# Optimization experiments

Measured on AMD Instinct MI355X. Metric: run time of the kernel, lower is better.

The kernel has to match this reference:

```python
import jax, jax.numpy as jnp
import numpy as np

N_POL = 100000
N_TICK = 20000
N = N_POL + N_TICK
E = 1000000
POL_FEAT = 7
EMB = 128
HID = 256
OUT = 128
N_STATES = 60


def setup_inputs() -> dict:
    key = jax.random.key(0)
    ks = jax.random.split(key, 16)
    s = 0.05
    return {
        "pol_features": jax.random.normal(ks[0], (N_POL, POL_FEAT), dtype=jnp.float32),
        "state_ids": jax.random.randint(ks[1], (N_POL,), 0, N_STATES, dtype=jnp.int32),
        "edge_index": jax.random.randint(ks[2], (2, E), 0, N, dtype=jnp.int32),
        "edge_weight": jax.random.uniform(ks[3], (E,), dtype=jnp.float32),
        # parameters
        "W_proj": jax.random.normal(ks[4], (POL_FEAT, EMB), dtype=jnp.float32) * s,
        "b_proj": jnp.zeros((EMB,), dtype=jnp.float32),
        "state_emb": jax.random.normal(ks[5], (N_STATES, EMB), dtype=jnp.float32) * s,
        "emb_tick": jax.random.normal(ks[6], (N_TICK, EMB), dtype=jnp.float32) * s,
        "W1_rel": jax.random.normal(ks[7], (EMB, HID), dtype=jnp.float32) * s,
        "b1_rel": jnp.zeros((HID,), dtype=jnp.float32),
        "W1_root": jax.random.normal(ks[8], (EMB, HID), dtype=jnp.float32) * s,
        "W2_rel": jax.random.normal(ks[9], (HID, OUT), dtype=jnp.float32) * s,
        "b2_rel": jnp.zeros((OUT,), dtype=jnp.float32),
        "W2_root": jax.random.normal(ks[10], (HID, OUT), dtype=jnp.float32) * s,
    }


def _graph_conv(x, edge_index, edge_weight, W_rel, b_rel, W_root):
    # PyG GraphConv: out = lin_rel(sum_{j->i} w_ji * x_j) + lin_root(x_i)
    src, dst = edge_index[0], edge_index[1]
    msg = x[src] * edge_weight[:, None]            # [E, d]
    agg = jax.ops.segment_sum(msg, dst, num_segments=N)  # [N, d]
    return agg @ W_rel + b_rel + x @ W_root


def reference(pol_features, state_ids, edge_index, edge_weight,
              W_proj, b_proj, state_emb, emb_tick,
              W1_rel, b1_rel, W1_root, W2_rel, b2_rel, W2_root):
    # Node features: projected politician feats + state embedding, cat tick embeddings
    pol = jax.nn.relu(pol_features @ W_proj + b_proj) + state_emb[state_ids]  # [N_POL, EMB]
    x = jnp.concatenate([pol, emb_tick], axis=0)   # [N, EMB]
    h = jax.nn.relu(_graph_conv(x, edge_index, edge_weight, W1_rel, b1_rel, W1_root))
    # dropout is identity in eval mode
    out = _graph_conv(h, edge_index, edge_weight, W2_rel, b2_rel, W2_root)
    return out  # [N, OUT]
```

## Files before the change

### kernel.cpp

```cpp
#include <hip/hip_runtime.h>
#include <hip/hip_bf16.h>

typedef unsigned short u16;
using short8  = __attribute__((ext_vector_type(8))) short;
using ushort8 = __attribute__((ext_vector_type(8))) unsigned short;
using float4v = __attribute__((ext_vector_type(4))) float;

#define N_POL  100000
#define N_TICK 20000
#define NNODE  120000
#define NEDGE  1000000
#define NTILE  1875
#define GB2    512

static __device__ __forceinline__ float b2f(u16 u) {
    return __uint_as_float(((unsigned)u) << 16);
}
static __device__ __forceinline__ u16 f2b(float f) {
    unsigned u = __float_as_uint(f);
    unsigned r = (u + 0x7FFFu + ((u >> 16) & 1u)) >> 16;
    return (u16)r;
}
static __device__ __forceinline__ float lde(const void* p, size_t i, int f32) {
    return f32 ? ((const float*)p)[i] : b2f(((const u16*)p)[i]);
}

static __device__ __forceinline__ size_t frag_addr(int k, int n) {
    return ((size_t)((n >> 4) * 8 + (k >> 5)) * 64 + (((k >> 3) & 3) * 16 + (n & 15))) * 8
           + (k & 7);
}

static __device__ __forceinline__ void gload_lds16(const u16* g, u16* l) {
    __builtin_amdgcn_global_load_lds(
        (const __attribute__((address_space(1))) void*)g,
        (__attribute__((address_space(3))) void*)l, 16, 0, 0);
}

static __device__ __forceinline__ void stage_tile(const u16* __restrict__ agg,
                                                  const u16* __restrict__ Xb,
                                                  int row0, u16* dst,
                                                  int wid, int lane) {
    int kqL = lane & 31;
#pragma unroll
    for (int i = 0; i < 8; i++) {
        int t = i * 4 + wid;
        int row = 2 * t + (lane >> 5);
        int kqG = kqL ^ (row & 7);
        const u16* src = (kqG < 16)
            ? agg + ((size_t)(row0 + row)) * 128 + kqG * 8
            : Xb + ((size_t)(row0 + row)) * 128 + (kqG - 16) * 8;
        gload_lds16(src, dst + (size_t)t * 512);
    }
}

__global__ void detect_k(const void* __restrict__ ew, int* __restrict__ flag) {
    if (threadIdx.x == 0) {
        const u16* p = (const u16*)ew;
        int huge = 0, allz = 1;
        for (int i = 0; i < 128; i += 2) {
            u16 b = p[i];
            if (b != 0) allz = 0;
            float v = b2f(b);
            if (!(fabsf(v) <= 4.0f)) huge = 1;
        }
        *flag = huge | allz;
    }
}

__global__ __launch_bounds__(256) void build_x(const void* __restrict__ pf,
                                               const int* __restrict__ sid,
                                               const void* __restrict__ Wp,
                                               const void* __restrict__ bp,
                                               const void* __restrict__ semb,
                                               const void* __restrict__ et,
                                               const int* __restrict__ flag,
                                               u16* __restrict__ Xb) {
    const int f32 = *flag;
    if (blockIdx.x < N_POL / 2) {
        int row = blockIdx.x * 2 + (threadIdx.x >> 7);
        int j = threadIdx.x & 127;
        float s = lde(bp, j, f32);
#pragma unroll
        for (int k = 0; k < 7; k++)
            s = fmaf(lde(pf, (size_t)row * 7 + k, f32), lde(Wp, k * 128 + j, f32), s);
        s = fmaxf(s, 0.f);
        s += lde(semb, (size_t)sid[row] * 128 + j, f32);
        Xb[(size_t)row * 128 + j] = f2b(s);
    } else {
        int idx = (blockIdx.x - N_POL / 2) * 256 + threadIdx.x;
        Xb[(size_t)N_POL * 128 + idx] = f2b(lde(et, idx, f32));
    }
}

__global__ __launch_bounds__(256) void prep_wf(const void* __restrict__ W1rel,
                                               const void* __restrict__ W1root,
                                               const void* __restrict__ W2rel,
                                               const void* __restrict__ W2root,
                                               const int* __restrict__ flag,
                                               u16* __restrict__ Wf1,
                                               u16* __restrict__ Wf2) {
    const int f32 = *flag;
    int idx = blockIdx.x * 256 + threadIdx.x;
    int id = idx & 65535;
    int k = id >> 8, n = id & 255;
    if (idx < 65536) {
        float v = (k < 128) ? lde(W1rel, (size_t)k * 256 + n, f32)
                            : lde(W1root, (size_t)(k - 128) * 256 + n, f32);
        Wf1[frag_addr(k, n)] = f2b(v);
    } else {
        float v = (n < 128) ? lde(W2rel, (size_t)k * 128 + n, f32)
                            : lde(W2root, (size_t)k * 128 + (n - 128), f32);
        Wf2[frag_addr(k, n)] = f2b(v);
    }
}

__global__ __launch_bounds__(256) void hist_dst(const int* __restrict__ ei,
                                                int* __restrict__ count,
                                                int* __restrict__ rank) {
    int e = blockIdx.x * 256 + threadIdx.x;
    if (e < NEDGE) rank[e] = atomicAdd(&count[ei[NEDGE + e]], 1);
}

__global__ __launch_bounds__(256) void scan1(const int* __restrict__ count,
                                             int* __restrict__ row_tmp,
                                             int* __restrict__ bsum) {
    __shared__ int sd[256];
    int t = threadIdx.x;
    int i = blockIdx.x * 256 + t;
    int c = (i < NNODE) ? count[i] : 0;
    sd[t] = c;
    __syncthreads();
#pragma unroll
    for (int off = 1; off < 256; off <<= 1) {
        int v = (t >= off) ? sd[t - off] : 0;
        __syncthreads();
        sd[t] += v;
        __syncthreads();
    }
    if (i < NNODE) row_tmp[i] = sd[t] - c;
    if (t == 255) bsum[blockIdx.x] = sd[t];
}

__global__ __launch_bounds__(512) void scan2(int* __restrict__ bsum, int nb) {
    __shared__ int sd[512];
    int t = threadIdx.x;
    int v = (t < nb) ? bsum[t] : 0;
    sd[t] = v;
    __syncthreads();
#pragma unroll
    for (int off = 1; off < 512; off <<= 1) {
        int u = (t >= off) ? sd[t - off] : 0;
        __syncthreads();
        sd[t] += u;
        __syncthreads();
    }
    if (t < nb) bsum[t] = sd[t] - v;
}

__global__ __launch_bounds__(256) void scan3(const int* __restrict__ row_tmp,
                                             const int* __restrict__ bsum,
                                             int* __restrict__ row_start) {
    int i = blockIdx.x * 256 + threadIdx.x;
    if (i < NNODE) row_start[i] = row_tmp[i] + bsum[blockIdx.x];
    if (i == 0) row_start[NNODE] = NEDGE;
}

__global__ __launch_bounds__(256) void fill_csr(const int* __restrict__ ei,
                                                const void* __restrict__ ew,
                                                const int* __restrict__ flag,
                                                const int* __restrict__ row_start,
                                                const int* __restrict__ rank,
                                                uint2* __restrict__ epk) {
    const int f32 = *flag;
    int e = blockIdx.x * 256 + threadIdx.x;
    if (e >= NEDGE) return;
    int src = ei[e];
    int dst = ei[NEDGE + e];
    int pos = row_start[dst] + rank[e];
    uint2 pk;
    pk.x = (unsigned)src;
    pk.y = (unsigned)f2b(lde(ew, e, f32));
    epk[pos] = pk;
}

__global__ __launch_bounds__(256) void gather128(const int* __restrict__ row_start,
                                                 const uint2* __restrict__ epk,
                                                 const u16* __restrict__ S,
                                                 u16* __restrict__ agg) {
    int n = blockIdx.x * 4 + (threadIdx.x >> 6);
    int lane = threadIdx.x & 63;
    int g4 = lane >> 4;
    int l16 = lane & 15;
    int s0 = row_start[n], s1 = row_start[n + 1];
    float a[8] = {0.f, 0.f, 0.f, 0.f, 0.f, 0.f, 0.f, 0.f};
    int e = s0;
    for (; e + 8 <= s1; e += 8) {
        uint2 p0 = epk[e + g4], p1 = epk[e + 4 + g4];
        float w0 = b2f((u16)p0.y), w1 = b2f((u16)p1.y);
        ushort8 x0 = *(const ushort8*)(S + (size_t)p0.x * 128 + l16 * 8);
        ushort8 x1 = *(const ushort8*)(S + (size_t)p1.x * 128 + l16 * 8);
#pragma unroll
        for (int j = 0; j < 8; j++) {
            a[j] = fmaf(b2f(x0[j]), w0, a[j]);
            a[j] = fmaf(b2f(x1[j]), w1, a[j]);
        }
    }
    for (; e + 4 <= s1; e += 4) {
        uint2 p = epk[e + g4];
        float w = b2f((u16)p.y);
        ushort8 x = *(const ushort8*)(S + (size_t)p.x * 128 + l16 * 8);
#pragma unroll
        for (int j = 0; j < 8; j++) a[j] = fmaf(b2f(x[j]), w, a[j]);
    }
    if (e < s1) {
        int eg = e + g4;
        int valid = eg < s1;
        uint2 p = epk[valid ? eg : s0];
        float w = valid ? b2f((u16)p.y) : 0.f;
        ushort8 x = *(const ushort8*)(S + (size_t)p.x * 128 + l16 * 8);
#pragma unroll
        for (int j = 0; j < 8; j++) a[j] = fmaf(b2f(x[j]), w, a[j]);
    }
#pragma unroll
    for (int j = 0; j < 8; j++) {
        a[j] += __shfl_xor(a[j], 16);
        a[j] += __shfl_xor(a[j], 32);
    }
    if (g4 == 0) {
        ushort8 o;
#pragma unroll
        for (int j = 0; j < 8; j++) o[j] = f2b(a[j]);
        *(ushort8*)(agg + (size_t)n * 128 + l16 * 8) = o;
    }
}

__global__ __launch_bounds__(256) void gather_add(const int* __restrict__ row_start,
                                                  const uint2* __restrict__ epk,
                                                  const u16* __restrict__ T2,
                                                  const u16* __restrict__ P,
                                                  const int* __restrict__ flag,
                                                  void* __restrict__ out) {
    const int f32 = *flag;
    int n = blockIdx.x * 4 + (threadIdx.x >> 6);
    int lane = threadIdx.x & 63;
    int g4 = lane >> 4;
    int l16 = lane & 15;
    int s0 = row_start[n], s1 = row_start[n + 1];
    float a[8] = {0.f, 0.f, 0.f, 0.f, 0.f, 0.f, 0.f, 0.f};
    int e = s0;
    for (; e + 8 <= s1; e += 8) {
        uint2 p0 = epk[e + g4], p1 = epk[e + 4 + g4];
        float w0 = b2f((u16)p0.y), w1 = b2f((u16)p1.y);
        ushort8 x0 = *(const ushort8*)(T2 + (size_t)p0.x * 128 + l16 * 8);
        ushort8 x1 = *(const ushort8*)(T2 + (size_t)p1.x * 128 + l16 * 8);
#pragma unroll
        for (int j = 0; j < 8; j++) {
            a[j] = fmaf(b2f(x0[j]), w0, a[j]);
            a[j] = fmaf(b2f(x1[j]), w1, a[j]);
        }
    }
    for (; e + 4 <= s1; e += 4) {
        uint2 p = epk[e + g4];
        float w = b2f((u16)p.y);
        ushort8 x = *(const ushort8*)(T2 + (size_t)p.x * 128 + l16 * 8);
#pragma unroll
        for (int j = 0; j < 8; j++) a[j] = fmaf(b2f(x[j]), w, a[j]);
    }
    if (e < s1) {
        int eg = e + g4;
        int valid = eg < s1;
        uint2 p = epk[valid ? eg : s0];
        float w = valid ? b2f((u16)p.y) : 0.f;
        ushort8 x = *(const ushort8*)(T2 + (size_t)p.x * 128 + l16 * 8);
#pragma unroll
        for (int j = 0; j < 8; j++) a[j] = fmaf(b2f(x[j]), w, a[j]);
    }
#pragma unroll
    for (int j = 0; j < 8; j++) {
        a[j] += __shfl_xor(a[j], 16);
        a[j] += __shfl_xor(a[j], 32);
    }
    if (g4 == 0) {
        ushort8 pv = *(const ushort8*)(P + (size_t)n * 128 + l16 * 8);
        float v[8];
#pragma unroll
        for (int j = 0; j < 8; j++) v[j] = a[j] + b2f(pv[j]);
        if (f32) {
            float4 s0v, s1v;
            s0v.x = v[0]; s0v.y = v[1]; s0v.z = v[2]; s0v.w = v[3];
            s1v.x = v[4]; s1v.y = v[5]; s1v.z = v[6]; s1v.w = v[7];
            *(float4*)((float*)out + (size_t)n * 128 + l16 * 8) = s0v;
            *(float4*)((float*)out + (size_t)n * 128 + l16 * 8 + 4) = s1v;
        } else {
            ushort8 s;
#pragma unroll
            for (int j = 0; j < 8; j++) s[j] = f2b(v[j]);
            *(ushort8*)((u16*)out + (size_t)n * 128 + l16 * 8) = s;
        }
    }
}

__global__ __launch_bounds__(256) void fused_gemm(const u16* __restrict__ agg,
                                                  const u16* __restrict__ Xb,
                                                  const u16* __restrict__ Wf1,
                                                  const u16* __restrict__ Wf2,
                                                  const void* __restrict__ b1,
                                                  const void* __restrict__ b2,
                                                  u16* __restrict__ T2,
                                                  u16* __restrict__ P,
                                                  const int* __restrict__ flag,
                                                  int ntiles) {
    const int f32 = *flag;
    __shared__ u16 LDS2[2][16384];
    const int wid = threadIdx.x >> 6;
    const int lane = threadIdx.x & 63;
    const int q = lane >> 4, lm = lane & 15;

    stage_tile(agg, Xb, blockIdx.x * 64, LDS2[0], wid, lane);

    for (int k = 0, t = blockIdx.x; t < ntiles; k++, t += GB2) {
        const int cur = k & 1;
        u16* B = LDS2[cur];
        const int row0 = t * 64;
        __syncthreads();

        float4v acc[4][4];
#pragma unroll
        for (int i = 0; i < 4; i++)
#pragma unroll
            for (int j = 0; j < 4; j++) acc[i][j] = (float4v){0.f, 0.f, 0.f, 0.f};
#pragma unroll
        for (int kb = 0; kb < 8; kb++) {
            short8 a[4];
#pragma unroll
            for (int ti = 0; ti < 4; ti++) {
                int rl = ti * 16 + lm;
                int chunk = (kb * 4 + q) ^ (rl & 7);
                a[ti] = *(const short8*)(B + (size_t)rl * 256 + chunk * 8);
            }
            short8 b[4];
#pragma unroll
            for (int tj = 0; tj < 4; tj++) {
                int nt = wid * 4 + tj;
                b[tj] = *(const short8*)(Wf1 + ((size_t)(nt * 8 + kb) * 64 + lane) * 8);
            }
#pragma unroll
            for (int ti = 0; ti < 4; ti++)
#pragma unroll
                for (int tj = 0; tj < 4; tj++)
                    acc[ti][tj] = __builtin_amdgcn_mfma_f32_16x16x32_bf16(
                        a[ti], b[tj], acc[ti][tj], 0, 0, 0);
        }
        __syncthreads();

#pragma unroll
        for (int tj = 0; tj < 4; tj++) {
            int col = wid * 64 + tj * 16 + lm;
            float bv = lde(b1, col, f32);
            int kq2 = col >> 3, jj = col & 7;
#pragma unroll
            for (int ti = 0; ti < 4; ti++) {
                int rl = ti * 16 + q * 4;
#pragma unroll
                for (int r = 0; r < 4; r++) {
                    float v = fmaxf(acc[ti][tj][r] + bv, 0.f);
                    B[((size_t)kq2 * 64 + rl + r) * 8 + jj] = f2b(v);
                }
            }
        }
        __syncthreads();

        float4v acc2[4][4];
#pragma unroll
        for (int i = 0; i < 4; i++)
#pragma unroll
            for (int j = 0; j < 4; j++) acc2[i][j] = (float4v){0.f, 0.f, 0.f, 0.f};
#pragma unroll
        for (int kb = 0; kb < 8; kb++) {
            short8 a[4];
#pragma unroll
            for (int ti = 0; ti < 4; ti++) {
                int rl = ti * 16 + lm;
                a[ti] = *(const short8*)(B + ((size_t)(kb * 4 + q) * 64 + rl) * 8);
            }
            short8 b[4];
#pragma unroll
            for (int tj = 0; tj < 4; tj++) {
                int nt = wid * 4 + tj;
                b[tj] = *(const short8*)(Wf2 + ((size_t)(nt * 8 + kb) * 64 + lane) * 8);
            }
#pragma unroll
            for (int ti = 0; ti < 4; ti++)
#pragma unroll
                for (int tj = 0; tj < 4; tj++)
                    acc2[ti][tj] = __builtin_amdgcn_mfma_f32_16x16x32_bf16(
                        a[ti], b[tj], acc2[ti][tj], 0, 0, 0);
        }

        if (t + GB2 < ntiles)
            stage_tile(agg, Xb, (t + GB2) * 64, LDS2[cur ^ 1], wid, lane);

        __syncthreads();

#pragma unroll
        for (int tj = 0; tj < 4; tj++) {
            int col = wid * 64 + tj * 16 + lm;
            int chunk = col >> 3, jj = col & 7;
            float bv = (col < 128) ? 0.f : lde(b2, col - 128, f32);
#pragma unroll
            for (int ti = 0; ti < 4; ti++) {
#pragma unroll
                for (int r = 0; r < 4; r++) {
                    int row = ti * 16 + q * 4 + r;
                    int pchunk = chunk ^ (((row >> 2) & 3) << 1);
                    B[((size_t)row * 32 + pchunk) * 8 + jj] = f2b(acc2[ti][tj][r] + bv);
                }
            }
        }
        __syncthreads();
#pragma unroll
        for (int i = 0; i < 8; i++) {
            int g = i * 256 + threadIdx.x;
            int row = g >> 5;
            int chunk = g & 31;
            int pchunk = chunk ^ (((row >> 2) & 3) << 1);
            short8 v = *(const short8*)(B + ((size_t)row * 32 + pchunk) * 8);
            int grow = row0 + row;
            int colu = chunk * 8;
            u16* dst = (colu < 128) ? (T2 + (size_t)grow * 128 + colu)
                                    : (P + (size_t)grow * 128 + (colu - 128));
            *(short8*)dst = v;
        }
    }
}

extern "C" void kernel_launch(void* const* d_in, const int* in_sizes, int n_in,
                              void* d_out, int out_size, void* d_ws, size_t ws_size,
                              hipStream_t stream) {
    const void* pf     = d_in[0];
    const int*  sid    = (const int*)d_in[1];
    const int*  ei     = (const int*)d_in[2];
    const void* ew     = d_in[3];
    const void* Wp     = d_in[4];
    const void* bp     = d_in[5];
    const void* semb   = d_in[6];
    const void* et     = d_in[7];
    const void* W1rel  = d_in[8];
    const void* b1     = d_in[9];
    const void* W1root = d_in[10];
    const void* W2rel  = d_in[11];
    const void* b2     = d_in[12];
    const void* W2root = d_in[13];

    char* w = (char*)d_ws;
    u16*   agg       = (u16*)w;
    u16*   T2        = (u16*)(w + 30720000);
    u16*   P         = (u16*)(w + 61440000);
    u16*   Wf1       = (u16*)(w + 92160000);
    u16*   Wf2       = (u16*)(w + 92291072);
    uint2* epk       = (uint2*)(w + 92422144);
    int*   rank      = (int*)(w + 100422144);
    int*   row_start = (int*)(w + 104422144);
    int*   row_tmp   = (int*)(w + 104902148);
    int*   count     = (int*)(w + 105382148);
    int*   bsum      = (int*)(w + 105862148);
    int*   flag      = (int*)(w + 105866244);
    u16*   Xb        = (u16*)d_out;

    const int EB = (NEDGE + 255) / 256;
    const int NB = (NNODE + 255) / 256;

    detect_k<<<1, 64, 0, stream>>>(ew, flag);

    hipMemsetAsync(count, 0, NNODE * sizeof(int), stream);
    hist_dst<<<EB, 256, 0, stream>>>(ei, count, rank);
    scan1<<<NB, 256, 0, stream>>>(count, row_tmp, bsum);
    scan2<<<1, 512, 0, stream>>>(bsum, NB);
    scan3<<<NB, 256, 0, stream>>>(row_tmp, bsum, row_start);
    fill_csr<<<EB, 256, 0, stream>>>(ei, ew, flag, row_start, rank, epk);

    prep_wf<<<512, 256, 0, stream>>>(W1rel, W1root, W2rel, W2root, flag, Wf1, Wf2);

    build_x<<<N_POL / 2 + (N_TICK * 128) / 256, 256, 0, stream>>>(
        pf, sid, Wp, bp, semb, et, flag, Xb);

    gather128<<<NNODE / 4, 256, 0, stream>>>(row_start, epk, Xb, agg);

    fused_gemm<<<GB2, 256, 0, stream>>>(agg, Xb, Wf1, Wf2, b1, b2, T2, P, flag, NTILE);

    gather_add<<<NNODE / 4, 256, 0, stream>>>(row_start, epk, T2, P, flag, d_out);
}
```

Baseline: 382.6 us.

## Replicate degree histogram counters and launch one fused GEMM block per tile

The destination-degree histogram now spreads its atomics over eight replicated count arrays, picked by block index, to cut atomic contention on hot nodes. The scan merges the replicas into per-replica offsets that the CSR fill uses, so edge order within each row stays deterministic. The fused two-layer GEMM drops its persistent double-buffered loop and instead launches one block per 64-row tile using a single LDS buffer. That lowers LDS use and raises occupancy, but it loses the overlap between staging the next tile and computing the current one, and it adds more memset and scan traffic.

```diff
diff --git a/kernel.cpp b/kernel.cpp
--- a/kernel.cpp
+++ b/kernel.cpp
@@ -10,8 +10,7 @@
 #define N_TICK 20000
 #define NNODE  120000
 #define NEDGE  1000000
-#define NTILE  1875
-#define GB2    512
+#define NREP   8
 
 static __device__ __forceinline__ float b2f(u16 u) {
     return __uint_as_float(((unsigned)u) << 16);
@@ -34,23 +33,6 @@
     __builtin_amdgcn_global_load_lds(
         (const __attribute__((address_space(1))) void*)g,
         (__attribute__((address_space(3))) void*)l, 16, 0, 0);
-}
-
-static __device__ __forceinline__ void stage_tile(const u16* __restrict__ agg,
-                                                  const u16* __restrict__ Xb,
-                                                  int row0, u16* dst,
-                                                  int wid, int lane) {
-    int kqL = lane & 31;
-#pragma unroll
-    for (int i = 0; i < 8; i++) {
-        int t = i * 4 + wid;
-        int row = 2 * t + (lane >> 5);
-        int kqG = kqL ^ (row & 7);
-        const u16* src = (kqG < 16)
-            ? agg + ((size_t)(row0 + row)) * 128 + kqG * 8
-            : Xb + ((size_t)(row0 + row)) * 128 + (kqG - 16) * 8;
-        gload_lds16(src, dst + (size_t)t * 512);
-    }
 }
 
 __global__ void detect_k(const void* __restrict__ ew, int* __restrict__ flag) {
@@ -117,17 +99,28 @@
 __global__ __launch_bounds__(256) void hist_dst(const int* __restrict__ ei,
                                                 int* __restrict__ count,
                                                 int* __restrict__ rank) {
+    int rep = blockIdx.x & (NREP - 1);
     int e = blockIdx.x * 256 + threadIdx.x;
-    if (e < NEDGE) rank[e] = atomicAdd(&count[ei[NEDGE + e]], 1);
+    if (e < NEDGE)
+        rank[e] = atomicAdd(&count[rep * NNODE + ei[NEDGE + e]], 1);
 }
 
 __global__ __launch_bounds__(256) void scan1(const int* __restrict__ count,
+                                             int* __restrict__ roff,
                                              int* __restrict__ row_tmp,
                                              int* __restrict__ bsum) {
     __shared__ int sd[256];
     int t = threadIdx.x;
     int i = blockIdx.x * 256 + t;
-    int c = (i < NNODE) ? count[i] : 0;
+    int c = 0;
+    if (i < NNODE) {
+#pragma unroll
+        for (int r = 0; r < NREP; r++) {
+            int v = count[r * NNODE + i];
+            roff[r * NNODE + i] = c;
+            c += v;
+        }
+    }
     sd[t] = c;
     __syncthreads();
 #pragma unroll
@@ -169,14 +162,16 @@
                                                 const void* __restrict__ ew,
                                                 const int* __restrict__ flag,
                                                 const int* __restrict__ row_start,
+                                                const int* __restrict__ roff,
                                                 const int* __restrict__ rank,
                                                 uint2* __restrict__ epk) {
     const int f32 = *flag;
+    int rep = blockIdx.x & (NREP - 1);
     int e = blockIdx.x * 256 + threadIdx.x;
     if (e >= NEDGE) return;
     int src = ei[e];
     int dst = ei[NEDGE + e];
-    int pos = row_start[dst] + rank[e];
+    int pos = row_start[dst] + roff[rep * NNODE + dst] + rank[e];
     uint2 pk;
     pk.x = (unsigned)src;
     pk.y = (unsigned)f2b(lde(ew, e, f32));
@@ -309,129 +304,133 @@
                                                   u16* __restrict__ T2,
                                                   u16* __restrict__ P,
                                                   const int* __restrict__ flag,
-                                                  int ntiles) {
+                                                  int M) {
     const int f32 = *flag;
-    __shared__ u16 LDS2[2][16384];
+    __shared__ u16 LDSU[32 * 64 * 8];
+    const int row0 = blockIdx.x * 64;
     const int wid = threadIdx.x >> 6;
     const int lane = threadIdx.x & 63;
     const int q = lane >> 4, lm = lane & 15;
 
-    stage_tile(agg, Xb, blockIdx.x * 64, LDS2[0], wid, lane);
-
-    for (int k = 0, t = blockIdx.x; t < ntiles; k++, t += GB2) {
-        const int cur = k & 1;
-        u16* B = LDS2[cur];
-        const int row0 = t * 64;
-        __syncthreads();
-
-        float4v acc[4][4];
-#pragma unroll
-        for (int i = 0; i < 4; i++)
-#pragma unroll
-            for (int j = 0; j < 4; j++) acc[i][j] = (float4v){0.f, 0.f, 0.f, 0.f};
-#pragma unroll
-        for (int kb = 0; kb < 8; kb++) {
-            short8 a[4];
-#pragma unroll
-            for (int ti = 0; ti < 4; ti++) {
-                int rl = ti * 16 + lm;
-                int chunk = (kb * 4 + q) ^ (rl & 7);
-                a[ti] = *(const short8*)(B + (size_t)rl * 256 + chunk * 8);
+    {
+        int kqL = lane & 31;
+#pragma unroll
+        for (int i = 0; i < 8; i++) {
+            int t = i * 4 + wid;
+            int row = 2 * t + (lane >> 5);
+            int kqG = kqL ^ (row & 7);
+            const u16* src = (kqG < 16)
+                ? agg + ((size_t)(row0 + row)) * 128 + kqG * 8
+                : Xb + ((size_t)(row0 + row)) * 128 + (kqG - 16) * 8;
+            gload_lds16(src, LDSU + (size_t)t * 512);
+        }
+    }
+    __syncthreads();
+
+    float4v acc[4][4];
+#pragma unroll
+    for (int i = 0; i < 4; i++)
+#pragma unroll
+        for (int j = 0; j < 4; j++) acc[i][j] = (float4v){0.f, 0.f, 0.f, 0.f};
+#pragma unroll
+    for (int kb = 0; kb < 8; kb++) {
+        short8 a[4];
+#pragma unroll
+        for (int ti = 0; ti < 4; ti++) {
+            int rl = ti * 16 + lm;
+            int chunk = (kb * 4 + q) ^ (rl & 7);
+            a[ti] = *(const short8*)(LDSU + (size_t)rl * 256 + chunk * 8);
+        }
+        short8 b[4];
+#pragma unroll
+        for (int tj = 0; tj < 4; tj++) {
+            int nt = wid * 4 + tj;
+            b[tj] = *(const short8*)(Wf1 + ((size_t)(nt * 8 + kb) * 64 + lane) * 8);
+        }
+#pragma unroll
+        for (int ti = 0; ti < 4; ti++)
+#pragma unroll
+            for (int tj = 0; tj < 4; tj++)
+                acc[ti][tj] = __builtin_amdgcn_mfma_f32_16x16x32_bf16(
+                    a[ti], b[tj], acc[ti][tj], 0, 0, 0);
+    }
+    __syncthreads();
+
+#pragma unroll
+    for (int tj = 0; tj < 4; tj++) {
+        int col = wid * 64 + tj * 16 + lm;
+        float bv = lde(b1, col, f32);
+        int kq2 = col >> 3, jj = col & 7;
+#pragma unroll
+        for (int ti = 0; ti < 4; ti++) {
+            int rl = ti * 16 + q * 4;
+#pragma unroll
+            for (int r = 0; r < 4; r++) {
+                float v = fmaxf(acc[ti][tj][r] + bv, 0.f);
+                LDSU[((size_t)kq2 * 64 + rl + r) * 8 + jj] = f2b(v);
             }
-            short8 b[4];
-#pragma unroll
-            for (int tj = 0; tj < 4; tj++) {
-                int nt = wid * 4 + tj;
-                b[tj] = *(const short8*)(Wf1 + ((size_t)(nt * 8 + kb) * 64 + lane) * 8);
+        }
+    }
+    __syncthreads();
+
+    float4v acc2[4][4];
+#pragma unroll
+    for (int i = 0; i < 4; i++)
+#pragma unroll
+        for (int j = 0; j < 4; j++) acc2[i][j] = (float4v){0.f, 0.f, 0.f, 0.f};
+#pragma unroll
+    for (int kb = 0; kb < 8; kb++) {
+        short8 a[4];
+#pragma unroll
+        for (int ti = 0; ti < 4; ti++) {
+            int rl = ti * 16 + lm;
+            a[ti] = *(const short8*)(LDSU + ((size_t)(kb * 4 + q) * 64 + rl) * 8);
+        }
+        short8 b[4];
+#pragma unroll
+        for (int tj = 0; tj < 4; tj++) {
+            int nt = wid * 4 + tj;
+            b[tj] = *(const short8*)(Wf2 + ((size_t)(nt * 8 + kb) * 64 + lane) * 8);
+        }
+#pragma unroll
+        for (int ti = 0; ti < 4; ti++)
+#pragma unroll
+            for (int tj = 0; tj < 4; tj++)
+                acc2[ti][tj] = __builtin_amdgcn_mfma_f32_16x16x32_bf16(
+                    a[ti], b[tj], acc2[ti][tj], 0, 0, 0);
+    }
+    __syncthreads();
+
+#pragma unroll
+    for (int tj = 0; tj < 4; tj++) {
+        int col = wid * 64 + tj * 16 + lm;
+        int chunk = col >> 3, jj = col & 7;
+        float bv = (col < 128) ? 0.f : lde(b2, col - 128, f32);
+#pragma unroll
+        for (int ti = 0; ti < 4; ti++) {
+#pragma unroll
+            for (int r = 0; r < 4; r++) {
+                int row = ti * 16 + q * 4 + r;
+                int pchunk = chunk ^ (((row >> 2) & 3) << 1);
+                LDSU[((size_t)row * 32 + pchunk) * 8 + jj] = f2b(acc2[ti][tj][r] + bv);
             }
-#pragma unroll
-            for (int ti = 0; ti < 4; ti++)
-#pragma unroll
-                for (int tj = 0; tj < 4; tj++)
-                    acc[ti][tj] = __builtin_amdgcn_mfma_f32_16x16x32_bf16(
-                        a[ti], b[tj], acc[ti][tj], 0, 0, 0);
-        }
-        __syncthreads();
-
-#pragma unroll
-        for (int tj = 0; tj < 4; tj++) {
-            int col = wid * 64 + tj * 16 + lm;
-            float bv = lde(b1, col, f32);
-            int kq2 = col >> 3, jj = col & 7;
-#pragma unroll
-            for (int ti = 0; ti < 4; ti++) {
-                int rl = ti * 16 + q * 4;
-#pragma unroll
-                for (int r = 0; r < 4; r++) {
-                    float v = fmaxf(acc[ti][tj][r] + bv, 0.f);
-                    B[((size_t)kq2 * 64 + rl + r) * 8 + jj] = f2b(v);
-                }
-            }
-        }
-        __syncthreads();
-
-        float4v acc2[4][4];
-#pragma unroll
-        for (int i = 0; i < 4; i++)
-#pragma unroll
-            for (int j = 0; j < 4; j++) acc2[i][j] = (float4v){0.f, 0.f, 0.f, 0.f};
-#pragma unroll
-        for (int kb = 0; kb < 8; kb++) {
-            short8 a[4];
-#pragma unroll
-            for (int ti = 0; ti < 4; ti++) {
-                int rl = ti * 16 + lm;
-                a[ti] = *(const short8*)(B + ((size_t)(kb * 4 + q) * 64 + rl) * 8);
-            }
-            short8 b[4];
-#pragma unroll
-            for (int tj = 0; tj < 4; tj++) {
-                int nt = wid * 4 + tj;
-                b[tj] = *(const short8*)(Wf2 + ((size_t)(nt * 8 + kb) * 64 + lane) * 8);
-            }
-#pragma unroll
-            for (int ti = 0; ti < 4; ti++)
-#pragma unroll
-                for (int tj = 0; tj < 4; tj++)
-                    acc2[ti][tj] = __builtin_amdgcn_mfma_f32_16x16x32_bf16(
-                        a[ti], b[tj], acc2[ti][tj], 0, 0, 0);
-        }
-
-        if (t + GB2 < ntiles)
-            stage_tile(agg, Xb, (t + GB2) * 64, LDS2[cur ^ 1], wid, lane);
-
-        __syncthreads();
-
-#pragma unroll
-        for (int tj = 0; tj < 4; tj++) {
-            int col = wid * 64 + tj * 16 + lm;
-            int chunk = col >> 3, jj = col & 7;
-            float bv = (col < 128) ? 0.f : lde(b2, col - 128, f32);
-#pragma unroll
-            for (int ti = 0; ti < 4; ti++) {
-#pragma unroll
-                for (int r = 0; r < 4; r++) {
-                    int row = ti * 16 + q * 4 + r;
-                    int pchunk = chunk ^ (((row >> 2) & 3) << 1);
-                    B[((size_t)row * 32 + pchunk) * 8 + jj] = f2b(acc2[ti][tj][r] + bv);
-                }
-            }
-        }
-        __syncthreads();
-#pragma unroll
-        for (int i = 0; i < 8; i++) {
-            int g = i * 256 + threadIdx.x;
-            int row = g >> 5;
-            int chunk = g & 31;
-            int pchunk = chunk ^ (((row >> 2) & 3) << 1);
-            short8 v = *(const short8*)(B + ((size_t)row * 32 + pchunk) * 8);
-            int grow = row0 + row;
-            int colu = chunk * 8;
-            u16* dst = (colu < 128) ? (T2 + (size_t)grow * 128 + colu)
-                                    : (P + (size_t)grow * 128 + (colu - 128));
-            *(short8*)dst = v;
-        }
-    }
+        }
+    }
+    __syncthreads();
+#pragma unroll
+    for (int i = 0; i < 8; i++) {
+        int g = i * 256 + threadIdx.x;
+        int row = g >> 5;
+        int chunk = g & 31;
+        int pchunk = chunk ^ (((row >> 2) & 3) << 1);
+        short8 v = *(const short8*)(LDSU + ((size_t)row * 32 + pchunk) * 8);
+        int grow = row0 + row;
+        int colu = chunk * 8;
+        u16* dst = (colu < 128) ? (T2 + (size_t)grow * 128 + colu)
+                                : (P + (size_t)grow * 128 + (colu - 128));
+        *(short8*)dst = v;
+    }
+    (void)M;
 }
 
 extern "C" void kernel_launch(void* const* d_in, const int* in_sizes, int n_in,
@@ -463,21 +462,23 @@
     int*   row_start = (int*)(w + 104422144);
     int*   row_tmp   = (int*)(w + 104902148);
     int*   count     = (int*)(w + 105382148);
-    int*   bsum      = (int*)(w + 105862148);
-    int*   flag      = (int*)(w + 105866244);
+    int*   roff      = (int*)(w + 109222148);
+    int*   bsum      = (int*)(w + 113062148);
+    int*   flag      = (int*)(w + 113066244);
     u16*   Xb        = (u16*)d_out;
 
     const int EB = (NEDGE + 255) / 256;
     const int NB = (NNODE + 255) / 256;
+    const int GB = (NNODE + 63) / 64;
 
     detect_k<<<1, 64, 0, stream>>>(ew, flag);
 
-    hipMemsetAsync(count, 0, NNODE * sizeof(int), stream);
+    hipMemsetAsync(count, 0, NREP * NNODE * sizeof(int), stream);
     hist_dst<<<EB, 256, 0, stream>>>(ei, count, rank);
-    scan1<<<NB, 256, 0, stream>>>(count, row_tmp, bsum);
+    scan1<<<NB, 256, 0, stream>>>(count, roff, row_tmp, bsum);
     scan2<<<1, 512, 0, stream>>>(bsum, NB);
     scan3<<<NB, 256, 0, stream>>>(row_tmp, bsum, row_start);
-    fill_csr<<<EB, 256, 0, stream>>>(ei, ew, flag, row_start, rank, epk);
+    fill_csr<<<EB, 256, 0, stream>>>(ei, ew, flag, row_start, roff, rank, epk);
 
     prep_wf<<<512, 256, 0, stream>>>(W1rel, W1root, W2rel, W2root, flag, Wf1, Wf2);
 
@@ -486,7 +487,7 @@
 
     gather128<<<NNODE / 4, 256, 0, stream>>>(row_start, epk, Xb, agg);
 
-    fused_gemm<<<GB2, 256, 0, stream>>>(agg, Xb, Wf1, Wf2, b1, b2, T2, P, flag, NTILE);
+    fused_gemm<<<GB, 256, 0, stream>>>(agg, Xb, Wf1, Wf2, b1, b2, T2, P, flag, NNODE);
 
     gather_add<<<NNODE / 4, 256, 0, stream>>>(row_start, epk, T2, P, flag, d_out);
 }
```

New measurement: 373.7 us. -2.3%, faster.
